# Kernel tuning notes

Hardware: AMD Instinct MI355X
Metric: run time of the kernel (lower is better)

The kernel has to match this reference:

```python
import jax, jax.numpy as jnp
import numpy as np

N_QUBITS = 20
N_LAYERS = 4
BATCH = 16
DIM = 2 ** N_QUBITS


def _apply_ry(state, theta, q, n):
    """Apply RY(theta) = [[cos(t/2), -sin(t/2)], [sin(t/2), cos(t/2)]] on qubit q.
    state: (B, 2**n) complex. Qubit 0 is most significant (qibo convention)."""
    c = jnp.cos(theta / 2).astype(state.dtype)
    s = jnp.sin(theta / 2).astype(state.dtype)
    B = state.shape[0]
    st = state.reshape(B, 2 ** q, 2, 2 ** (n - q - 1))
    a = st[:, :, 0, :]
    b = st[:, :, 1, :]
    new = jnp.stack([c * a - s * b, s * a + c * b], axis=2)
    return new.reshape(B, -1)


def _apply_cnot(state, cq, tq, n):
    """CNOT with control cq < target tq: flip target bit where control bit is 1."""
    B = state.shape[0]
    st = state.reshape(B, 2 ** cq, 2, 2 ** (tq - cq - 1), 2, 2 ** (n - tq - 1))
    ctrl0 = st[:, :, 0]                      # (B, 2^cq, mid, 2, rest)
    ctrl1 = jnp.flip(st[:, :, 1], axis=3)    # swap target |0>/<->|1>
    new = jnp.stack([ctrl0, ctrl1], axis=2)
    return new.reshape(B, -1)


def _run_circuit(state, theta):
    # theta: (N_LAYERS * N_QUBITS,) -> (N_LAYERS, N_QUBITS)
    th = theta.reshape(N_LAYERS, N_QUBITS)
    for l in range(N_LAYERS):
        for q in range(N_QUBITS):
            state = _apply_ry(state, th[l, q], q, N_QUBITS)
        for q in range(N_QUBITS - 1):
            state = _apply_cnot(state, q, q + 1, N_QUBITS)
    return state


def setup_inputs() -> dict:
    key = jax.random.key(0)
    k1, k2 = jax.random.split(key)
    x = jax.random.normal(k1, (BATCH, DIM), dtype=jnp.float32)
    theta = jax.random.normal(k2, (N_LAYERS * N_QUBITS,), dtype=jnp.float32)
    return {"x": x, "theta": theta}


def reference(x, theta):
    state = x.astype(jnp.complex64)  # initial state vector, (B, 2**n)
    state = _run_circuit(state, theta)
    return jnp.abs(state)
```

## Files before the change

kernel.cpp:

```cpp
#include <hip/hip_runtime.h>
#include <math.h>


__global__ void cs_kernel(const float* __restrict__ theta, float2* __restrict__ cs) {
    int i = threadIdx.x;
    if (i < 80) {
        float s, c;
        sincosf(theta[i] * 0.5f, &s, &c);
        cs[i] = make_float2(c, s);
    }
}

#define RYT_(TBL, MASK, Q) { float2 _sc = (TBL)[(Q)]; float _c = _sc.x, _s = _sc.y; \
  _Pragma("unroll") for (int _m = 0; _m < 32; ++_m) if (!(_m & (MASK))) { \
    float _a = v[_m], _b = v[_m | (MASK)]; \
    v[_m] = _c*_a - _s*_b; v[_m | (MASK)] = _s*_a + _c*_b; } }

#define CX_(CM, TM) { _Pragma("unroll") for (int _m = 0; _m < 32; ++_m) \
  if ((_m & (CM)) && !(_m & (TM))) { float _t = v[_m]; v[_m] = v[_m|(TM)]; v[_m|(TM)] = _t; } }

#define CXI_(COND, TM) { if (COND) { _Pragma("unroll") for (int _m = 0; _m < 32; ++_m) \
  if (!(_m & (TM))) { float _t = v[_m]; v[_m] = v[_m|(TM)]; v[_m|(TM)] = _t; } } }

__device__ __forceinline__ int mixR(int n) {
    return ((n >> 5) & 31) ^ ((n >> 10) & 1);
}
__device__ __forceinline__ int mixA(int n) {
    return ((n >> 5) & 31) ^ ((n >> 10) & 1) ^ (((n >> 11) & 1) << 3)
         ^ (((n >> 12) & 1) << 4) ^ (((n >> 13) & 1) << 4);
}
__device__ __forceinline__ int mixF(int n) {
    return ((n >> 5) & 31) ^ (((n >> 10) & 1) << 1) ^ (((n >> 11) & 1) << 2)
         ^ (((n >> 12) & 1) << 3) ^ (((n >> 13) & 1) << 4);
}
__device__ __forceinline__ int mixL(int n) {
    return ((n >> 5) & 31) ^ (((n >> 10) & 1) << 4) ^ (((n >> 11) & 1) << 2)
         ^ (((n >> 12) & 1) << 3) ^ (((n >> 13) & 1) << 4);
}

__global__ __launch_bounds__(512, 4) void pass_R(
    const float4* __restrict__ src, float4* __restrict__ dst,
    const float2* __restrict__ cs)
{
    __shared__ float lds[16384];
    const float2* csl = cs;
    int t = threadIdx.x, blk = blockIdx.x;
    int H = blk & 63, b = blk >> 6;
    int base = (b << 18) + (H << 12);
    float v[32];

#pragma unroll
    for (int i = 0; i < 8; ++i) {
        float4 w = src[base + (i << 8) + (((t >> 6) & 3) << 6) + (((t >> 8) & 1) << 11) + (t & 63)];
        v[i*4+0] = w.x; v[i*4+1] = w.y; v[i*4+2] = w.z; v[i*4+3] = w.w;
    }
    RYT_(csl, 1, 19); RYT_(csl, 2, 18); RYT_(csl, 4, 9); RYT_(csl, 8, 8); RYT_(csl, 16, 7);
    { int w1x = (t & 31) ^ ((t >> 5) & 1);
#pragma unroll
      for (int m = 0; m < 32; ++m) lds[(t << 5) | (m ^ w1x)] = v[m]; }
    __syncthreads();

    { int tp = (t & 31) | (((t >> 5) & 1) << 10) | (((t >> 6) & 7) << 11);
      int mt = mixR(tp);
#pragma unroll
      for (int f = 0; f < 32; ++f) { int fc = f << 5; v[f] = lds[(tp | fc) ^ mt ^ mixR(fc)]; }
      RYT_(csl, 1, 17); RYT_(csl, 2, 16); RYT_(csl, 4, 15); RYT_(csl, 8, 14); RYT_(csl, 16, 13);
#pragma unroll
      for (int f = 0; f < 32; ++f) { int fc = f << 5; lds[(tp | fc) ^ mt ^ mixR(fc)] = v[f]; } }
    __syncthreads();

    { int tp = ((t & 1) << 2) | (((t >> 1) & 1) << 3) | (((t >> 2) & 1) << 4)
             | (((t >> 3) & 1) << 5) | (((t >> 4) & 1) << 1) | (((t >> 5) & 1) << 0)
             | (((t >> 6) & 7) << 6);
      int mt = mixR(tp);
#pragma unroll
      for (int p = 0; p < 32; ++p) { int fc = p << 9; v[p] = lds[(tp | fc) ^ mt ^ mixR(fc)]; }
      RYT_(csl, 2, 12); RYT_(csl, 4, 11); RYT_(csl, 8, 10); RYT_(csl, 16, 6);
      int sb = base + (((t >> 6) & 7) << 6) + (t & 63);
#pragma unroll
      for (int j = 0; j < 8; ++j)
        dst[sb + (j << 9)] = make_float4(v[4*j], v[4*j+1], v[4*j+2], v[4*j+3]); }
}

template <bool FULL>
__global__ __launch_bounds__(512, 4) void pass_A(
    const float4* __restrict__ src, float4* __restrict__ dst,
    const float2* __restrict__ cs, int layer)
{
    __shared__ float lds[16384];
    const float2* csl = cs + layer * 20;
    int t = threadIdx.x, blk = blockIdx.x;
    int G = blk & 63, b = blk >> 6;
    int Gperm = ((G >> 2) & 1) | (((G >> 1) & 1) << 1) | ((G & 1) << 2) | (((G >> 3) & 7) << 3);
    float v[32];

    { int lb = (b << 18) + (((t >> 6) & 7) << 9) + (Gperm << 3) + (t & 7);
      int rg = ((t >> 3) & 7) << 12;
#pragma unroll
      for (int i = 0; i < 8; ++i) {
        float4 w = src[lb + ((i << 3) << 12) + rg];
        v[i*4+0] = w.x; v[i*4+1] = w.y; v[i*4+2] = w.z; v[i*4+3] = w.w;
      } }
    RYT_(csl, 16, 0); RYT_(csl, 8, 1); RYT_(csl, 4, 2);
    if (FULL) { RYT_(csl, 2, 12); RYT_(csl, 1, 13); }
    { int w1x = (t & 31) ^ ((t >> 5) & 1) ^ (((t >> 6) & 1) << 3)
              ^ (((t >> 7) & 1) << 4) ^ (((t >> 8) & 1) << 4);
#pragma unroll
      for (int m = 0; m < 32; ++m) lds[(t << 5) | (m ^ w1x)] = v[m]; }
    __syncthreads();

    { int tp = (t & 3) | (((t >> 2) & 1) << 7) | (((t >> 3) & 1) << 11)
             | (((t >> 4) & 1) << 12) | (((t >> 5) & 1) << 13) | (((t >> 6) & 1) << 5)
             | (((t >> 7) & 1) << 6) | (((t >> 8) & 1) << 8);
      int mt = mixA(tp);
#pragma unroll
      for (int f = 0; f < 32; ++f) {
        int fc = ((f & 1) << 9) | (((f >> 1) & 1) << 10) | (((f >> 2) & 1) << 2)
               | (((f >> 3) & 1) << 3) | (((f >> 4) & 1) << 4);
        v[f] = lds[(tp | fc) ^ mt ^ mixA(fc)]; }
      RYT_(csl, 1, 4); RYT_(csl, 2, 3);
      CX_(16, 8); CX_(8, 4); CX_(4, 2); CX_(2, 1);
#pragma unroll
      for (int f = 0; f < 32; ++f) {
        int fc = ((f & 1) << 9) | (((f >> 1) & 1) << 10) | (((f >> 2) & 1) << 2)
               | (((f >> 3) & 1) << 3) | (((f >> 4) & 1) << 4);
        lds[(tp | fc) ^ mt ^ mixA(fc)] = v[f]; } }
    __syncthreads();

    { int tp = (t & 31) | (((t >> 5) & 1) << 9) | (((t >> 6) & 1) << 10)
             | (((t >> 7) & 1) << 11) | (((t >> 8) & 1) << 12);
      int mt = mixA(tp);
#pragma unroll
      for (int f = 0; f < 32; ++f) {
        int fc = ((f & 1) << 5) | (((f >> 1) & 1) << 6) | (((f >> 2) & 1) << 7)
               | (((f >> 3) & 1) << 13) | (((f >> 4) & 1) << 8);
        v[f] = lds[(tp | fc) ^ mt ^ mixA(fc)]; }
      RYT_(csl, 16, 5);
      if (FULL) { RYT_(csl, 8, 6); RYT_(csl, 4, 7); RYT_(csl, 2, 8); RYT_(csl, 1, 9); }
      CXI_((t >> 5) & 1, 16); CX_(16, 8); CX_(8, 4); CX_(4, 2); CX_(2, 1);
#pragma unroll
      for (int f = 0; f < 32; ++f) {
        int fc = ((f & 1) << 5) | (((f >> 1) & 1) << 6) | (((f >> 2) & 1) << 7)
               | (((f >> 3) & 1) << 13) | (((f >> 4) & 1) << 8);
        lds[(tp | fc) ^ mt ^ mixA(fc)] = v[f]; } }
    __syncthreads();

    { int tp = ((t & 1) << 8) | (((t >> 1) & 1) << 9) | (((t >> 2) & 1) << 10)
             | (((t >> 3) & 1) << 6) | (((t >> 4) & 1) << 7) | (((t >> 5) & 1) << 2)
             | (((t >> 6) & 1) << 5) | (((t >> 7) & 1) << 3) | (((t >> 8) & 1) << 4);
      int mt = mixA(tp);
#pragma unroll
      for (int p = 0; p < 32; ++p) {
        int fc = ((p & 1) << 0) | (((p >> 1) & 1) << 13) | (((p >> 2) & 1) << 1)
               | (((p >> 3) & 1) << 11) | (((p >> 4) & 1) << 12);
        v[p] = lds[(tp | fc) ^ mt ^ mixA(fc)]; }
      if (FULL) { RYT_(csl, 16, 10); RYT_(csl, 8, 11); }
      CXI_((t >> 6) & 1, 16); CX_(16, 8); CX_(8, 4); CX_(4, 1);
      int sb = (b << 18) + (G << 12) + t;
#pragma unroll
      for (int j = 0; j < 8; ++j)
        dst[sb + (j << 9)] = make_float4(v[4*j], v[4*j+1], v[4*j+2], v[4*j+3]); }
}

template <bool LOWRY>
__global__ __launch_bounds__(512, 4) void pass_F(
    const float4* __restrict__ src, float4* __restrict__ dst,
    const float2* __restrict__ cs, int layer)
{
    __shared__ float lds[16384];
    const float2* csl  = cs + layer * 20;
    const float2* csl2 = cs + (layer + 1) * 20;
    int t = threadIdx.x, blk = blockIdx.x;
    int W = blk & 63, b = blk >> 6;
    int Wp = (((W >> 4) & 1) << 3) | (((W >> 5) & 1) << 4) | (((W >> 3) & 1) << 6)
           | ((W & 1) << 9) | (((W >> 1) & 1) << 10) | (((W >> 2) & 1) << 11);
    float v[32];

    { int lb = (((b << 6) | ((t >> 3) & 63)) << 12) + (t & 7) + Wp;
#pragma unroll
      for (int i = 0; i < 8; ++i) {
        float4 w = src[lb + ((i & 1) << 5) + (((i >> 1) & 1) << 7) + (((i >> 2) & 1) << 8)];
        v[i*4+0] = w.x; v[i*4+1] = w.y; v[i*4+2] = w.z; v[i*4+3] = w.w;
      } }
    RYT_(csl2, 16, 0); RYT_(csl2, 8, 1); RYT_(csl2, 4, 2); RYT_(csl2, 2, 6);
    CX_(16, 8); CX_(8, 4);
    { int w1x = (t & 31) ^ (((t >> 5) & 1) << 1) ^ (((t >> 6) & 1) << 2)
              ^ (((t >> 7) & 1) << 3) ^ (((t >> 8) & 1) << 4);
#pragma unroll
      for (int m = 0; m < 32; ++m) lds[(t << 5) | (m ^ w1x)] = v[m]; }
    __syncthreads();

    { int tp = (t & 31) | (((t >> 5) & 1) << 8) | (((t >> 6) & 1) << 5)
             | (((t >> 7) & 1) << 6) | (((t >> 8) & 1) << 7);
      int mt = mixF(tp);
#pragma unroll
      for (int f = 0; f < 32; ++f) { int fc = f << 9; v[f] = lds[(tp | fc) ^ mt ^ mixF(fc)]; }
      if (LOWRY) { RYT_(csl, 16, 14); RYT_(csl, 8, 15); RYT_(csl, 4, 16); RYT_(csl, 2, 17); RYT_(csl, 1, 18); }
      CXI_(t & 1, 16); CX_(16, 8); CX_(8, 4); CX_(4, 2); CX_(2, 1);
#pragma unroll
      for (int f = 0; f < 32; ++f) { int fc = f << 9; lds[(tp | fc) ^ mt ^ mixF(fc)] = v[f]; } }
    __syncthreads();

    { int tp = ((t & 1) << 12) | (((t >> 1) & 1) << 13) | (((t >> 2) & 1) << 0)
             | (((t >> 3) & 1) << 9) | (((t >> 4) & 1) << 10) | (((t >> 5) & 1) << 11)
             | (((t >> 6) & 1) << 2) | (((t >> 7) & 1) << 3) | (((t >> 8) & 1) << 4);
      int mt = mixF(tp);
#pragma unroll
      for (int p = 0; p < 32; ++p) {
        int fc = ((p & 1) << 8) | (((p >> 1) & 1) << 1) | (((p >> 2) & 1) << 5)
               | (((p >> 3) & 1) << 6) | (((p >> 4) & 1) << 7);
        v[p] = lds[(tp | fc) ^ mt ^ mixF(fc)]; }
      if (LOWRY) { RYT_(csl, 1, 19); }
      CXI_((t >> 3) & 1, 1);
      RYT_(csl2, 16, 3); RYT_(csl2, 8, 4); RYT_(csl2, 4, 5);
      CXI_((t >> 6) & 1, 16); CX_(16, 8); CX_(8, 4); CX_(4, 2);
      int sb = (blk << 12) + t;
#pragma unroll
      for (int j = 0; j < 8; ++j)
        dst[sb + (j << 9)] = make_float4(v[4*j], v[4*j+1], v[4*j+2], v[4*j+3]); }
}

template <bool FIN>
__global__ __launch_bounds__(512, 4) void pass_L(
    const float4* __restrict__ src, float4* __restrict__ dst,
    const float2* __restrict__ cs, int layer)
{
    __shared__ float lds[16384];
    const float2* csl = cs + layer * 20;
    int t = threadIdx.x, blk = blockIdx.x;
    int H = blk & 63, b = blk >> 6;
    int Hp = (((H >> 3) & 7) << 6) | ((H & 7) << 9);
    float v[32];

    { int rb = (b << 6) | ((t >> 6) & 7);
      int lo = Hp + (t & 63);
#pragma unroll
      for (int i = 0; i < 8; ++i) {
        float4 w = src[((rb | (i << 3)) << 12) + lo];
        v[i*4+0] = w.x; v[i*4+1] = w.y; v[i*4+2] = w.z; v[i*4+3] = w.w;
      } }
    RYT_(csl, 1, 19); RYT_(csl, 4, 9); RYT_(csl, 8, 8); RYT_(csl, 16, 7);
    { int w1x = (t & 31) ^ (((t >> 5) & 1) << 4) ^ (((t >> 6) & 1) << 2)
              ^ (((t >> 7) & 1) << 3) ^ (((t >> 8) & 1) << 4);
#pragma unroll
      for (int m = 0; m < 32; ++m) lds[(t << 5) | (m ^ w1x)] = v[m]; }
    __syncthreads();

    { int tp = (t & 3) | (((t >> 2) & 1) << 7) | (((t >> 3) & 1) << 8)
             | (((t >> 4) & 1) << 9) | (((t >> 5) & 1) << 10) | (((t >> 6) & 1) << 5)
             | (((t >> 7) & 1) << 6) | (((t >> 8) & 1) << 11);
      int mt = mixL(tp);
#pragma unroll
      for (int f = 0; f < 32; ++f) {
        int fc = ((f & 1) << 12) | (((f >> 1) & 1) << 13) | (((f >> 2) & 1) << 2)
               | (((f >> 3) & 1) << 3) | (((f >> 4) & 1) << 4);
        v[f] = lds[(tp | fc) ^ mt ^ mixL(fc)]; }
      RYT_(csl, 2, 10); RYT_(csl, 1, 11);
      CXI_((t >> 1) & 1, 16); CX_(16, 8); CX_(8, 4); CX_(4, 2); CX_(2, 1);
#pragma unroll
      for (int f = 0; f < 32; ++f) {
        int fc = ((f & 1) << 12) | (((f >> 1) & 1) << 13) | (((f >> 2) & 1) << 2)
               | (((f >> 3) & 1) << 3) | (((f >> 4) & 1) << 4);
        lds[(tp | fc) ^ mt ^ mixL(fc)] = v[f]; } }
    __syncthreads();

    { int tp = (t & 31) | (((t >> 5) & 1) << 9) | (((t >> 6) & 1) << 8)
             | (((t >> 7) & 1) << 12) | (((t >> 8) & 1) << 13);
      int mt = mixL(tp);
#pragma unroll
      for (int f = 0; f < 32; ++f) {
        int fc = ((f & 1) << 10) | (((f >> 1) & 1) << 5) | (((f >> 2) & 1) << 6)
               | (((f >> 3) & 1) << 7) | (((f >> 4) & 1) << 11);
        v[f] = lds[(tp | fc) ^ mt ^ mixL(fc)]; }
      RYT_(csl, 16, 12); RYT_(csl, 8, 13); RYT_(csl, 4, 14); RYT_(csl, 2, 15); RYT_(csl, 1, 16);
      CXI_((t >> 7) & 1, 16); CX_(16, 8); CX_(8, 4); CX_(4, 2); CX_(2, 1);
#pragma unroll
      for (int f = 0; f < 32; ++f) {
        int fc = ((f & 1) << 10) | (((f >> 1) & 1) << 5) | (((f >> 2) & 1) << 6)
               | (((f >> 3) & 1) << 7) | (((f >> 4) & 1) << 11);
        lds[(tp | fc) ^ mt ^ mixL(fc)] = v[f]; } }
    __syncthreads();

    { int tp;
      if (!FIN)
        tp = ((t & 1) << 2) | (((t >> 1) & 1) << 3) | (((t >> 2) & 1) << 4)
           | (((t >> 3) & 1) << 10) | (((t >> 4) & 1) << 5) | (((t >> 5) & 1) << 6)
           | (((t >> 6) & 1) << 1) | (((t >> 7) & 1) << 12) | (((t >> 8) & 1) << 13);
      else
        tp = ((t & 1) << 10) | (((t >> 1) & 1) << 5) | (((t >> 2) & 1) << 6)
           | (((t >> 3) & 1) << 12) | (((t >> 4) & 1) << 13) | (((t >> 5) & 1) << 2)
           | (((t >> 6) & 1) << 1) | (((t >> 7) & 1) << 3) | (((t >> 8) & 1) << 4);
      int mt = mixL(tp);
#pragma unroll
      for (int u = 0; u < 32; ++u) {
        int fc = ((u & 1) << 0) | (((u >> 1) & 1) << 8) | (((u >> 2) & 1) << 9)
               | (((u >> 3) & 1) << 7) | (((u >> 4) & 1) << 11);
        v[u] = lds[(tp | fc) ^ mt ^ mixL(fc)]; }
      RYT_(csl, 4, 17); RYT_(csl, 2, 18);
      { int e3 = FIN ? (t & 1) : ((t >> 3) & 1);
        CXI_(e3, 4); }
      CX_(4, 2); CX_(2, 1);
      if (!FIN) {
        int sb = (blk << 12) + (t & 7) + (((t >> 3) & 7) << 6)
               + (((t >> 7) & 3) << 9) + (((t >> 6) & 1) << 11);
#pragma unroll
        for (int g = 0; g < 8; ++g) {
          int bu = ((g >> 2) & 1) | (((g >> 1) & 1) << 1) | ((g & 1) << 2);
          dst[sb + (g << 3)] = make_float4(v[bu], v[bu | 8], v[bu | 16], v[bu | 24]);
        }
      } else {
        int sb = (blk << 12) + ((t & 7) << 1) + (((t >> 3) & 7) << 6)
               + (((t >> 7) & 1) << 9) + (((t >> 8) & 1) << 10) + (((t >> 6) & 1) << 11);
#pragma unroll
        for (int g = 0; g < 8; ++g) {
          int bu = ((g & 1) << 2) | (((g >> 1) & 1) << 3) | (((g >> 2) & 1) << 4);
          dst[sb + (g & 1) + (((g >> 1) & 1) << 4) + (((g >> 2) & 1) << 5)] =
            make_float4(fabsf(v[bu]), fabsf(v[bu | 1]), fabsf(v[bu | 2]), fabsf(v[bu | 3]));
        }
      } }
}

extern "C" void kernel_launch(void* const* d_in, const int* in_sizes, int n_in,
                              void* d_out, int out_size, void* d_ws, size_t ws_size,
                              hipStream_t stream) {
    const float* x     = (const float*)d_in[0];
    const float* theta = (const float*)d_in[1];
    float2* cs = (float2*)d_ws;
    float4* wsS = (float4*)((char*)d_ws + 4096);
    float4* out = (float4*)d_out;

    cs_kernel<<<1, 128, 0, stream>>>(theta, cs);

    dim3 grid(1024), block(512);
    pass_R<<<grid, block, 0, stream>>>((const float4*)x, out, cs);
    pass_A<false><<<grid, block, 0, stream>>>(out, wsS, cs, 0);
    pass_F<false><<<grid, block, 0, stream>>>(wsS, out, cs, 0);
    pass_L<false><<<grid, block, 0, stream>>>(out, wsS, cs, 1);
    pass_A<true><<<grid, block, 0, stream>>>(wsS, out, cs, 2);
    pass_F<true><<<grid, block, 0, stream>>>(out, wsS, cs, 2);
    pass_L<true><<<grid, block, 0, stream>>>(wsS, out, cs, 3);
}
```

Before: 282.1 us.

## Process two tiles per block with early prefetch of second tile

Each block now handles two 16K-element tiles: it issues global loads for both tiles up front, then runs the LDS transpose phases for the first tile while the second tile's loads are in flight, and the grid is halved to 512 blocks. __syncthreads is replaced by an explicit lgkmcnt wait plus s_barrier, so the barrier does not also wait on outstanding global loads. The intent is to hide global memory latency behind LDS work. In exchange, register pressure roughly doubles (64 floats held per thread) under launch_bounds(512,4), which risks spilling or lower occupancy, and there are fewer blocks to spread across the CUs.

```diff
diff --git a/kernel.cpp b/kernel.cpp
--- a/kernel.cpp
+++ b/kernel.cpp
@@ -11,16 +11,18 @@
     }
 }
 
-#define RYT_(TBL, MASK, Q) { float2 _sc = (TBL)[(Q)]; float _c = _sc.x, _s = _sc.y; \
+#define BAR() { asm volatile("s_waitcnt lgkmcnt(0)" ::: "memory"); __builtin_amdgcn_s_barrier(); }
+
+#define RYV_(V, TBL, MASK, Q) { float2 _sc = (TBL)[(Q)]; float _c = _sc.x, _s = _sc.y; \
   _Pragma("unroll") for (int _m = 0; _m < 32; ++_m) if (!(_m & (MASK))) { \
-    float _a = v[_m], _b = v[_m | (MASK)]; \
-    v[_m] = _c*_a - _s*_b; v[_m | (MASK)] = _s*_a + _c*_b; } }
-
-#define CX_(CM, TM) { _Pragma("unroll") for (int _m = 0; _m < 32; ++_m) \
-  if ((_m & (CM)) && !(_m & (TM))) { float _t = v[_m]; v[_m] = v[_m|(TM)]; v[_m|(TM)] = _t; } }
-
-#define CXI_(COND, TM) { if (COND) { _Pragma("unroll") for (int _m = 0; _m < 32; ++_m) \
-  if (!(_m & (TM))) { float _t = v[_m]; v[_m] = v[_m|(TM)]; v[_m|(TM)] = _t; } } }
+    float _a = (V)[_m], _b = (V)[_m | (MASK)]; \
+    (V)[_m] = _c*_a - _s*_b; (V)[_m | (MASK)] = _s*_a + _c*_b; } }
+
+#define CXV_(V, CM, TM) { _Pragma("unroll") for (int _m = 0; _m < 32; ++_m) \
+  if ((_m & (CM)) && !(_m & (TM))) { float _t = (V)[_m]; (V)[_m] = (V)[_m|(TM)]; (V)[_m|(TM)] = _t; } }
+
+#define CXIV_(V, COND, TM) { if (COND) { _Pragma("unroll") for (int _m = 0; _m < 32; ++_m) \
+  if (!(_m & (TM))) { float _t = (V)[_m]; (V)[_m] = (V)[_m|(TM)]; (V)[_m|(TM)] = _t; } } }
 
 __device__ __forceinline__ int mixR(int n) {
     return ((n >> 5) & 31) ^ ((n >> 10) & 1);
@@ -37,6 +39,34 @@
     return ((n >> 5) & 31) ^ (((n >> 10) & 1) << 4) ^ (((n >> 11) & 1) << 2)
          ^ (((n >> 12) & 1) << 3) ^ (((n >> 13) & 1) << 4);
 }
+
+#define R_LOAD(BLK, V) { int H = (BLK) & 63, b = (BLK) >> 6; \
+  int base = (b << 18) + (H << 12); \
+  _Pragma("unroll") for (int i = 0; i < 8; ++i) { \
+    float4 w = src[base + (i << 8) + (((t >> 6) & 3) << 6) + (((t >> 8) & 1) << 11) + (t & 63)]; \
+    (V)[i*4+0] = w.x; (V)[i*4+1] = w.y; (V)[i*4+2] = w.z; (V)[i*4+3] = w.w; } }
+
+#define R_PH1(V) { \
+  RYV_(V, csl, 1, 19); RYV_(V, csl, 2, 18); RYV_(V, csl, 4, 9); RYV_(V, csl, 8, 8); RYV_(V, csl, 16, 7); \
+  int w1x = (t & 31) ^ ((t >> 5) & 1); \
+  _Pragma("unroll") for (int m = 0; m < 32; ++m) lds[(t << 5) | (m ^ w1x)] = (V)[m]; }
+
+#define R_PH2(V) { int tp = (t & 31) | (((t >> 5) & 1) << 10) | (((t >> 6) & 7) << 11); \
+  int mt = mixR(tp); \
+  _Pragma("unroll") for (int f = 0; f < 32; ++f) { int fc = f << 5; (V)[f] = lds[(tp | fc) ^ mt ^ mixR(fc)]; } \
+  RYV_(V, csl, 1, 17); RYV_(V, csl, 2, 16); RYV_(V, csl, 4, 15); RYV_(V, csl, 8, 14); RYV_(V, csl, 16, 13); \
+  _Pragma("unroll") for (int f = 0; f < 32; ++f) { int fc = f << 5; lds[(tp | fc) ^ mt ^ mixR(fc)] = (V)[f]; } }
+
+#define R_PH3(V, BLK) { int tp = ((t & 1) << 2) | (((t >> 1) & 1) << 3) | (((t >> 2) & 1) << 4) \
+             | (((t >> 3) & 1) << 5) | (((t >> 4) & 1) << 1) | (((t >> 5) & 1) << 0) \
+             | (((t >> 6) & 7) << 6); \
+  int mt = mixR(tp); \
+  _Pragma("unroll") for (int p = 0; p < 32; ++p) { int fc = p << 9; (V)[p] = lds[(tp | fc) ^ mt ^ mixR(fc)]; } \
+  RYV_(V, csl, 2, 12); RYV_(V, csl, 4, 11); RYV_(V, csl, 8, 10); RYV_(V, csl, 16, 6); \
+  int H = (BLK) & 63, b = (BLK) >> 6; \
+  int sb = (b << 18) + (H << 12) + (((t >> 6) & 7) << 6) + (t & 63); \
+  _Pragma("unroll") for (int j = 0; j < 8; ++j) \
+    dst[sb + (j << 9)] = make_float4((V)[4*j], (V)[4*j+1], (V)[4*j+2], (V)[4*j+3]); }
 
 __global__ __launch_bounds__(512, 4) void pass_R(
     const float4* __restrict__ src, float4* __restrict__ dst,
@@ -44,43 +74,78 @@
 {
     __shared__ float lds[16384];
     const float2* csl = cs;
-    int t = threadIdx.x, blk = blockIdx.x;
-    int H = blk & 63, b = blk >> 6;
-    int base = (b << 18) + (H << 12);
-    float v[32];
-
-#pragma unroll
-    for (int i = 0; i < 8; ++i) {
-        float4 w = src[base + (i << 8) + (((t >> 6) & 3) << 6) + (((t >> 8) & 1) << 11) + (t & 63)];
-        v[i*4+0] = w.x; v[i*4+1] = w.y; v[i*4+2] = w.z; v[i*4+3] = w.w;
-    }
-    RYT_(csl, 1, 19); RYT_(csl, 2, 18); RYT_(csl, 4, 9); RYT_(csl, 8, 8); RYT_(csl, 16, 7);
-    { int w1x = (t & 31) ^ ((t >> 5) & 1);
-#pragma unroll
-      for (int m = 0; m < 32; ++m) lds[(t << 5) | (m ^ w1x)] = v[m]; }
-    __syncthreads();
-
-    { int tp = (t & 31) | (((t >> 5) & 1) << 10) | (((t >> 6) & 7) << 11);
-      int mt = mixR(tp);
-#pragma unroll
-      for (int f = 0; f < 32; ++f) { int fc = f << 5; v[f] = lds[(tp | fc) ^ mt ^ mixR(fc)]; }
-      RYT_(csl, 1, 17); RYT_(csl, 2, 16); RYT_(csl, 4, 15); RYT_(csl, 8, 14); RYT_(csl, 16, 13);
-#pragma unroll
-      for (int f = 0; f < 32; ++f) { int fc = f << 5; lds[(tp | fc) ^ mt ^ mixR(fc)] = v[f]; } }
-    __syncthreads();
-
-    { int tp = ((t & 1) << 2) | (((t >> 1) & 1) << 3) | (((t >> 2) & 1) << 4)
-             | (((t >> 3) & 1) << 5) | (((t >> 4) & 1) << 1) | (((t >> 5) & 1) << 0)
-             | (((t >> 6) & 7) << 6);
-      int mt = mixR(tp);
-#pragma unroll
-      for (int p = 0; p < 32; ++p) { int fc = p << 9; v[p] = lds[(tp | fc) ^ mt ^ mixR(fc)]; }
-      RYT_(csl, 2, 12); RYT_(csl, 4, 11); RYT_(csl, 8, 10); RYT_(csl, 16, 6);
-      int sb = base + (((t >> 6) & 7) << 6) + (t & 63);
-#pragma unroll
-      for (int j = 0; j < 8; ++j)
-        dst[sb + (j << 9)] = make_float4(v[4*j], v[4*j+1], v[4*j+2], v[4*j+3]); }
-}
+    int t = threadIdx.x;
+    int blk0 = blockIdx.x, blk1 = blockIdx.x + 512;
+    float va[32], vb[32];
+
+    R_LOAD(blk0, va); R_LOAD(blk1, vb);
+    R_PH1(va); BAR();
+    R_PH2(va); BAR();
+    R_PH3(va, blk0); BAR();
+    R_PH1(vb); BAR();
+    R_PH2(vb); BAR();
+    R_PH3(vb, blk1);
+}
+
+#define A_LOAD(BLK, V) { int G = (BLK) & 63, b = (BLK) >> 6; \
+  int Gperm = ((G >> 2) & 1) | (((G >> 1) & 1) << 1) | ((G & 1) << 2) | (((G >> 3) & 7) << 3); \
+  int lb = (b << 18) + (((t >> 6) & 7) << 9) + (Gperm << 3) + (t & 7); \
+  int rg = ((t >> 3) & 7) << 12; \
+  _Pragma("unroll") for (int i = 0; i < 8; ++i) { \
+    float4 w = src[lb + ((i << 3) << 12) + rg]; \
+    (V)[i*4+0] = w.x; (V)[i*4+1] = w.y; (V)[i*4+2] = w.z; (V)[i*4+3] = w.w; } }
+
+#define A_PH1(V) { \
+  RYV_(V, csl, 16, 0); RYV_(V, csl, 8, 1); RYV_(V, csl, 4, 2); \
+  if (FULL) { RYV_(V, csl, 2, 12); RYV_(V, csl, 1, 13); } \
+  int w1x = (t & 31) ^ ((t >> 5) & 1) ^ (((t >> 6) & 1) << 3) \
+          ^ (((t >> 7) & 1) << 4) ^ (((t >> 8) & 1) << 4); \
+  _Pragma("unroll") for (int m = 0; m < 32; ++m) lds[(t << 5) | (m ^ w1x)] = (V)[m]; }
+
+#define A_PH2(V) { int tp = (t & 3) | (((t >> 2) & 1) << 7) | (((t >> 3) & 1) << 11) \
+             | (((t >> 4) & 1) << 12) | (((t >> 5) & 1) << 13) | (((t >> 6) & 1) << 5) \
+             | (((t >> 7) & 1) << 6) | (((t >> 8) & 1) << 8); \
+  int mt = mixA(tp); \
+  _Pragma("unroll") for (int f = 0; f < 32; ++f) { \
+    int fc = ((f & 1) << 9) | (((f >> 1) & 1) << 10) | (((f >> 2) & 1) << 2) \
+           | (((f >> 3) & 1) << 3) | (((f >> 4) & 1) << 4); \
+    (V)[f] = lds[(tp | fc) ^ mt ^ mixA(fc)]; } \
+  RYV_(V, csl, 1, 4); RYV_(V, csl, 2, 3); \
+  CXV_(V, 16, 8); CXV_(V, 8, 4); CXV_(V, 4, 2); CXV_(V, 2, 1); \
+  _Pragma("unroll") for (int f = 0; f < 32; ++f) { \
+    int fc = ((f & 1) << 9) | (((f >> 1) & 1) << 10) | (((f >> 2) & 1) << 2) \
+           | (((f >> 3) & 1) << 3) | (((f >> 4) & 1) << 4); \
+    lds[(tp | fc) ^ mt ^ mixA(fc)] = (V)[f]; } }
+
+#define A_PH3(V) { int tp = (t & 31) | (((t >> 5) & 1) << 9) | (((t >> 6) & 1) << 10) \
+             | (((t >> 7) & 1) << 11) | (((t >> 8) & 1) << 12); \
+  int mt = mixA(tp); \
+  _Pragma("unroll") for (int f = 0; f < 32; ++f) { \
+    int fc = ((f & 1) << 5) | (((f >> 1) & 1) << 6) | (((f >> 2) & 1) << 7) \
+           | (((f >> 3) & 1) << 13) | (((f >> 4) & 1) << 8); \
+    (V)[f] = lds[(tp | fc) ^ mt ^ mixA(fc)]; } \
+  RYV_(V, csl, 16, 5); \
+  if (FULL) { RYV_(V, csl, 8, 6); RYV_(V, csl, 4, 7); RYV_(V, csl, 2, 8); RYV_(V, csl, 1, 9); } \
+  CXIV_(V, (t >> 5) & 1, 16); CXV_(V, 16, 8); CXV_(V, 8, 4); CXV_(V, 4, 2); CXV_(V, 2, 1); \
+  _Pragma("unroll") for (int f = 0; f < 32; ++f) { \
+    int fc = ((f & 1) << 5) | (((f >> 1) & 1) << 6) | (((f >> 2) & 1) << 7) \
+           | (((f >> 3) & 1) << 13) | (((f >> 4) & 1) << 8); \
+    lds[(tp | fc) ^ mt ^ mixA(fc)] = (V)[f]; } }
+
+#define A_PH4(V, BLK) { int tp = ((t & 1) << 8) | (((t >> 1) & 1) << 9) | (((t >> 2) & 1) << 10) \
+             | (((t >> 3) & 1) << 6) | (((t >> 4) & 1) << 7) | (((t >> 5) & 1) << 2) \
+             | (((t >> 6) & 1) << 5) | (((t >> 7) & 1) << 3) | (((t >> 8) & 1) << 4); \
+  int mt = mixA(tp); \
+  _Pragma("unroll") for (int p = 0; p < 32; ++p) { \
+    int fc = ((p & 1) << 0) | (((p >> 1) & 1) << 13) | (((p >> 2) & 1) << 1) \
+           | (((p >> 3) & 1) << 11) | (((p >> 4) & 1) << 12); \
+    (V)[p] = lds[(tp | fc) ^ mt ^ mixA(fc)]; } \
+  if (FULL) { RYV_(V, csl, 16, 10); RYV_(V, csl, 8, 11); } \
+  CXIV_(V, (t >> 6) & 1, 16); CXV_(V, 16, 8); CXV_(V, 8, 4); CXV_(V, 4, 1); \
+  int G = (BLK) & 63, b = (BLK) >> 6; \
+  int sb = (b << 18) + (G << 12) + t; \
+  _Pragma("unroll") for (int j = 0; j < 8; ++j) \
+    dst[sb + (j << 9)] = make_float4((V)[4*j], (V)[4*j+1], (V)[4*j+2], (V)[4*j+3]); }
 
 template <bool FULL>
 __global__ __launch_bounds__(512, 4) void pass_A(
@@ -89,78 +154,59 @@
 {
     __shared__ float lds[16384];
     const float2* csl = cs + layer * 20;
-    int t = threadIdx.x, blk = blockIdx.x;
-    int G = blk & 63, b = blk >> 6;
-    int Gperm = ((G >> 2) & 1) | (((G >> 1) & 1) << 1) | ((G & 1) << 2) | (((G >> 3) & 7) << 3);
-    float v[32];
-
-    { int lb = (b << 18) + (((t >> 6) & 7) << 9) + (Gperm << 3) + (t & 7);
-      int rg = ((t >> 3) & 7) << 12;
-#pragma unroll
-      for (int i = 0; i < 8; ++i) {
-        float4 w = src[lb + ((i << 3) << 12) + rg];
-        v[i*4+0] = w.x; v[i*4+1] = w.y; v[i*4+2] = w.z; v[i*4+3] = w.w;
-      } }
-    RYT_(csl, 16, 0); RYT_(csl, 8, 1); RYT_(csl, 4, 2);
-    if (FULL) { RYT_(csl, 2, 12); RYT_(csl, 1, 13); }
-    { int w1x = (t & 31) ^ ((t >> 5) & 1) ^ (((t >> 6) & 1) << 3)
-              ^ (((t >> 7) & 1) << 4) ^ (((t >> 8) & 1) << 4);
-#pragma unroll
-      for (int m = 0; m < 32; ++m) lds[(t << 5) | (m ^ w1x)] = v[m]; }
-    __syncthreads();
-
-    { int tp = (t & 3) | (((t >> 2) & 1) << 7) | (((t >> 3) & 1) << 11)
-             | (((t >> 4) & 1) << 12) | (((t >> 5) & 1) << 13) | (((t >> 6) & 1) << 5)
-             | (((t >> 7) & 1) << 6) | (((t >> 8) & 1) << 8);
-      int mt = mixA(tp);
-#pragma unroll
-      for (int f = 0; f < 32; ++f) {
-        int fc = ((f & 1) << 9) | (((f >> 1) & 1) << 10) | (((f >> 2) & 1) << 2)
-               | (((f >> 3) & 1) << 3) | (((f >> 4) & 1) << 4);
-        v[f] = lds[(tp | fc) ^ mt ^ mixA(fc)]; }
-      RYT_(csl, 1, 4); RYT_(csl, 2, 3);
-      CX_(16, 8); CX_(8, 4); CX_(4, 2); CX_(2, 1);
-#pragma unroll
-      for (int f = 0; f < 32; ++f) {
-        int fc = ((f & 1) << 9) | (((f >> 1) & 1) << 10) | (((f >> 2) & 1) << 2)
-               | (((f >> 3) & 1) << 3) | (((f >> 4) & 1) << 4);
-        lds[(tp | fc) ^ mt ^ mixA(fc)] = v[f]; } }
-    __syncthreads();
-
-    { int tp = (t & 31) | (((t >> 5) & 1) << 9) | (((t >> 6) & 1) << 10)
-             | (((t >> 7) & 1) << 11) | (((t >> 8) & 1) << 12);
-      int mt = mixA(tp);
-#pragma unroll
-      for (int f = 0; f < 32; ++f) {
-        int fc = ((f & 1) << 5) | (((f >> 1) & 1) << 6) | (((f >> 2) & 1) << 7)
-               | (((f >> 3) & 1) << 13) | (((f >> 4) & 1) << 8);
-        v[f] = lds[(tp | fc) ^ mt ^ mixA(fc)]; }
-      RYT_(csl, 16, 5);
-      if (FULL) { RYT_(csl, 8, 6); RYT_(csl, 4, 7); RYT_(csl, 2, 8); RYT_(csl, 1, 9); }
-      CXI_((t >> 5) & 1, 16); CX_(16, 8); CX_(8, 4); CX_(4, 2); CX_(2, 1);
-#pragma unroll
-      for (int f = 0; f < 32; ++f) {
-        int fc = ((f & 1) << 5) | (((f >> 1) & 1) << 6) | (((f >> 2) & 1) << 7)
-               | (((f >> 3) & 1) << 13) | (((f >> 4) & 1) << 8);
-        lds[(tp | fc) ^ mt ^ mixA(fc)] = v[f]; } }
-    __syncthreads();
-
-    { int tp = ((t & 1) << 8) | (((t >> 1) & 1) << 9) | (((t >> 2) & 1) << 10)
-             | (((t >> 3) & 1) << 6) | (((t >> 4) & 1) << 7) | (((t >> 5) & 1) << 2)
-             | (((t >> 6) & 1) << 5) | (((t >> 7) & 1) << 3) | (((t >> 8) & 1) << 4);
-      int mt = mixA(tp);
-#pragma unroll
-      for (int p = 0; p < 32; ++p) {
-        int fc = ((p & 1) << 0) | (((p >> 1) & 1) << 13) | (((p >> 2) & 1) << 1)
-               | (((p >> 3) & 1) << 11) | (((p >> 4) & 1) << 12);
-        v[p] = lds[(tp | fc) ^ mt ^ mixA(fc)]; }
-      if (FULL) { RYT_(csl, 16, 10); RYT_(csl, 8, 11); }
-      CXI_((t >> 6) & 1, 16); CX_(16, 8); CX_(8, 4); CX_(4, 1);
-      int sb = (b << 18) + (G << 12) + t;
-#pragma unroll
-      for (int j = 0; j < 8; ++j)
-        dst[sb + (j << 9)] = make_float4(v[4*j], v[4*j+1], v[4*j+2], v[4*j+3]); }
-}
+    int t = threadIdx.x;
+    int blk0 = blockIdx.x, blk1 = blockIdx.x + 512;
+    float va[32], vb[32];
+
+    A_LOAD(blk0, va); A_LOAD(blk1, vb);
+    A_PH1(va); BAR();
+    A_PH2(va); BAR();
+    A_PH3(va); BAR();
+    A_PH4(va, blk0); BAR();
+    A_PH1(vb); BAR();
+    A_PH2(vb); BAR();
+    A_PH3(vb); BAR();
+    A_PH4(vb, blk1);
+}
+
+#define F_LOAD(BLK, V) { int W = (BLK) & 63, b = (BLK) >> 6; \
+  int Wp = (((W >> 4) & 1) << 3) | (((W >> 5) & 1) << 4) | (((W >> 3) & 1) << 6) \
+         | ((W & 1) << 9) | (((W >> 1) & 1) << 10) | (((W >> 2) & 1) << 11); \
+  int lb = (((b << 6) | ((t >> 3) & 63)) << 12) + (t & 7) + Wp; \
+  _Pragma("unroll") for (int i = 0; i < 8; ++i) { \
+    float4 w = src[lb + ((i & 1) << 5) + (((i >> 1) & 1) << 7) + (((i >> 2) & 1) << 8)]; \
+    (V)[i*4+0] = w.x; (V)[i*4+1] = w.y; (V)[i*4+2] = w.z; (V)[i*4+3] = w.w; } }
+
+#define F_PH1(V) { \
+  RYV_(V, csl2, 16, 0); RYV_(V, csl2, 8, 1); RYV_(V, csl2, 4, 2); RYV_(V, csl2, 2, 6); \
+  CXV_(V, 16, 8); CXV_(V, 8, 4); \
+  int w1x = (t & 31) ^ (((t >> 5) & 1) << 1) ^ (((t >> 6) & 1) << 2) \
+          ^ (((t >> 7) & 1) << 3) ^ (((t >> 8) & 1) << 4); \
+  _Pragma("unroll") for (int m = 0; m < 32; ++m) lds[(t << 5) | (m ^ w1x)] = (V)[m]; }
+
+#define F_PH2(V) { int tp = (t & 31) | (((t >> 5) & 1) << 8) | (((t >> 6) & 1) << 5) \
+             | (((t >> 7) & 1) << 6) | (((t >> 8) & 1) << 7); \
+  int mt = mixF(tp); \
+  _Pragma("unroll") for (int f = 0; f < 32; ++f) { int fc = f << 9; (V)[f] = lds[(tp | fc) ^ mt ^ mixF(fc)]; } \
+  if (LOWRY) { RYV_(V, csl, 16, 14); RYV_(V, csl, 8, 15); RYV_(V, csl, 4, 16); RYV_(V, csl, 2, 17); RYV_(V, csl, 1, 18); } \
+  CXIV_(V, t & 1, 16); CXV_(V, 16, 8); CXV_(V, 8, 4); CXV_(V, 4, 2); CXV_(V, 2, 1); \
+  _Pragma("unroll") for (int f = 0; f < 32; ++f) { int fc = f << 9; lds[(tp | fc) ^ mt ^ mixF(fc)] = (V)[f]; } }
+
+#define F_PH3(V, BLK) { int tp = ((t & 1) << 12) | (((t >> 1) & 1) << 13) | (((t >> 2) & 1) << 0) \
+             | (((t >> 3) & 1) << 9) | (((t >> 4) & 1) << 10) | (((t >> 5) & 1) << 11) \
+             | (((t >> 6) & 1) << 2) | (((t >> 7) & 1) << 3) | (((t >> 8) & 1) << 4); \
+  int mt = mixF(tp); \
+  _Pragma("unroll") for (int p = 0; p < 32; ++p) { \
+    int fc = ((p & 1) << 8) | (((p >> 1) & 1) << 1) | (((p >> 2) & 1) << 5) \
+           | (((p >> 3) & 1) << 6) | (((p >> 4) & 1) << 7); \
+    (V)[p] = lds[(tp | fc) ^ mt ^ mixF(fc)]; } \
+  if (LOWRY) { RYV_(V, csl, 1, 19); } \
+  CXIV_(V, (t >> 3) & 1, 1); \
+  RYV_(V, csl2, 16, 3); RYV_(V, csl2, 8, 4); RYV_(V, csl2, 4, 5); \
+  CXIV_(V, (t >> 6) & 1, 16); CXV_(V, 16, 8); CXV_(V, 8, 4); CXV_(V, 4, 2); \
+  int sb = ((BLK) << 12) + t; \
+  _Pragma("unroll") for (int j = 0; j < 8; ++j) \
+    dst[sb + (j << 9)] = make_float4((V)[4*j], (V)[4*j+1], (V)[4*j+2], (V)[4*j+3]); }
 
 template <bool LOWRY>
 __global__ __launch_bounds__(512, 4) void pass_F(
@@ -170,55 +216,96 @@
     __shared__ float lds[16384];
     const float2* csl  = cs + layer * 20;
     const float2* csl2 = cs + (layer + 1) * 20;
-    int t = threadIdx.x, blk = blockIdx.x;
-    int W = blk & 63, b = blk >> 6;
-    int Wp = (((W >> 4) & 1) << 3) | (((W >> 5) & 1) << 4) | (((W >> 3) & 1) << 6)
-           | ((W & 1) << 9) | (((W >> 1) & 1) << 10) | (((W >> 2) & 1) << 11);
-    float v[32];
-
-    { int lb = (((b << 6) | ((t >> 3) & 63)) << 12) + (t & 7) + Wp;
-#pragma unroll
-      for (int i = 0; i < 8; ++i) {
-        float4 w = src[lb + ((i & 1) << 5) + (((i >> 1) & 1) << 7) + (((i >> 2) & 1) << 8)];
-        v[i*4+0] = w.x; v[i*4+1] = w.y; v[i*4+2] = w.z; v[i*4+3] = w.w;
-      } }
-    RYT_(csl2, 16, 0); RYT_(csl2, 8, 1); RYT_(csl2, 4, 2); RYT_(csl2, 2, 6);
-    CX_(16, 8); CX_(8, 4);
-    { int w1x = (t & 31) ^ (((t >> 5) & 1) << 1) ^ (((t >> 6) & 1) << 2)
-              ^ (((t >> 7) & 1) << 3) ^ (((t >> 8) & 1) << 4);
-#pragma unroll
-      for (int m = 0; m < 32; ++m) lds[(t << 5) | (m ^ w1x)] = v[m]; }
-    __syncthreads();
-
-    { int tp = (t & 31) | (((t >> 5) & 1) << 8) | (((t >> 6) & 1) << 5)
-             | (((t >> 7) & 1) << 6) | (((t >> 8) & 1) << 7);
-      int mt = mixF(tp);
-#pragma unroll
-      for (int f = 0; f < 32; ++f) { int fc = f << 9; v[f] = lds[(tp | fc) ^ mt ^ mixF(fc)]; }
-      if (LOWRY) { RYT_(csl, 16, 14); RYT_(csl, 8, 15); RYT_(csl, 4, 16); RYT_(csl, 2, 17); RYT_(csl, 1, 18); }
-      CXI_(t & 1, 16); CX_(16, 8); CX_(8, 4); CX_(4, 2); CX_(2, 1);
-#pragma unroll
-      for (int f = 0; f < 32; ++f) { int fc = f << 9; lds[(tp | fc) ^ mt ^ mixF(fc)] = v[f]; } }
-    __syncthreads();
-
-    { int tp = ((t & 1) << 12) | (((t >> 1) & 1) << 13) | (((t >> 2) & 1) << 0)
-             | (((t >> 3) & 1) << 9) | (((t >> 4) & 1) << 10) | (((t >> 5) & 1) << 11)
-             | (((t >> 6) & 1) << 2) | (((t >> 7) & 1) << 3) | (((t >> 8) & 1) << 4);
-      int mt = mixF(tp);
-#pragma unroll
-      for (int p = 0; p < 32; ++p) {
-        int fc = ((p & 1) << 8) | (((p >> 1) & 1) << 1) | (((p >> 2) & 1) << 5)
-               | (((p >> 3) & 1) << 6) | (((p >> 4) & 1) << 7);
-        v[p] = lds[(tp | fc) ^ mt ^ mixF(fc)]; }
-      if (LOWRY) { RYT_(csl, 1, 19); }
-      CXI_((t >> 3) & 1, 1);
-      RYT_(csl2, 16, 3); RYT_(csl2, 8, 4); RYT_(csl2, 4, 5);
-      CXI_((t >> 6) & 1, 16); CX_(16, 8); CX_(8, 4); CX_(4, 2);
-      int sb = (blk << 12) + t;
-#pragma unroll
-      for (int j = 0; j < 8; ++j)
-        dst[sb + (j << 9)] = make_float4(v[4*j], v[4*j+1], v[4*j+2], v[4*j+3]); }
-}
+    int t = threadIdx.x;
+    int blk0 = blockIdx.x, blk1 = blockIdx.x + 512;
+    float va[32], vb[32];
+
+    F_LOAD(blk0, va); F_LOAD(blk1, vb);
+    F_PH1(va); BAR();
+    F_PH2(va); BAR();
+    F_PH3(va, blk0); BAR();
+    F_PH1(vb); BAR();
+    F_PH2(vb); BAR();
+    F_PH3(vb, blk1);
+}
+
+#define L_LOAD(BLK, V) { int H = (BLK) & 63, b = (BLK) >> 6; \
+  int Hp = (((H >> 3) & 7) << 6) | ((H & 7) << 9); \
+  int rb = (b << 6) | ((t >> 6) & 7); \
+  int lo = Hp + (t & 63); \
+  _Pragma("unroll") for (int i = 0; i < 8; ++i) { \
+    float4 w = src[((rb | (i << 3)) << 12) + lo]; \
+    (V)[i*4+0] = w.x; (V)[i*4+1] = w.y; (V)[i*4+2] = w.z; (V)[i*4+3] = w.w; } }
+
+#define L_PH1(V) { \
+  RYV_(V, csl, 1, 19); RYV_(V, csl, 4, 9); RYV_(V, csl, 8, 8); RYV_(V, csl, 16, 7); \
+  int w1x = (t & 31) ^ (((t >> 5) & 1) << 4) ^ (((t >> 6) & 1) << 2) \
+          ^ (((t >> 7) & 1) << 3) ^ (((t >> 8) & 1) << 4); \
+  _Pragma("unroll") for (int m = 0; m < 32; ++m) lds[(t << 5) | (m ^ w1x)] = (V)[m]; }
+
+#define L_PH2(V) { int tp = (t & 3) | (((t >> 2) & 1) << 7) | (((t >> 3) & 1) << 8) \
+             | (((t >> 4) & 1) << 9) | (((t >> 5) & 1) << 10) | (((t >> 6) & 1) << 5) \
+             | (((t >> 7) & 1) << 6) | (((t >> 8) & 1) << 11); \
+  int mt = mixL(tp); \
+  _Pragma("unroll") for (int f = 0; f < 32; ++f) { \
+    int fc = ((f & 1) << 12) | (((f >> 1) & 1) << 13) | (((f >> 2) & 1) << 2) \
+           | (((f >> 3) & 1) << 3) | (((f >> 4) & 1) << 4); \
+    (V)[f] = lds[(tp | fc) ^ mt ^ mixL(fc)]; } \
+  RYV_(V, csl, 2, 10); RYV_(V, csl, 1, 11); \
+  CXIV_(V, (t >> 1) & 1, 16); CXV_(V, 16, 8); CXV_(V, 8, 4); CXV_(V, 4, 2); CXV_(V, 2, 1); \
+  _Pragma("unroll") for (int f = 0; f < 32; ++f) { \
+    int fc = ((f & 1) << 12) | (((f >> 1) & 1) << 13) | (((f >> 2) & 1) << 2) \
+           | (((f >> 3) & 1) << 3) | (((f >> 4) & 1) << 4); \
+    lds[(tp | fc) ^ mt ^ mixL(fc)] = (V)[f]; } }
+
+#define L_PH3(V) { int tp = (t & 31) | (((t >> 5) & 1) << 9) | (((t >> 6) & 1) << 8) \
+             | (((t >> 7) & 1) << 12) | (((t >> 8) & 1) << 13); \
+  int mt = mixL(tp); \
+  _Pragma("unroll") for (int f = 0; f < 32; ++f) { \
+    int fc = ((f & 1) << 10) | (((f >> 1) & 1) << 5) | (((f >> 2) & 1) << 6) \
+           | (((f >> 3) & 1) << 7) | (((f >> 4) & 1) << 11); \
+    (V)[f] = lds[(tp | fc) ^ mt ^ mixL(fc)]; } \
+  RYV_(V, csl, 16, 12); RYV_(V, csl, 8, 13); RYV_(V, csl, 4, 14); RYV_(V, csl, 2, 15); RYV_(V, csl, 1, 16); \
+  CXIV_(V, (t >> 7) & 1, 16); CXV_(V, 16, 8); CXV_(V, 8, 4); CXV_(V, 4, 2); CXV_(V, 2, 1); \
+  _Pragma("unroll") for (int f = 0; f < 32; ++f) { \
+    int fc = ((f & 1) << 10) | (((f >> 1) & 1) << 5) | (((f >> 2) & 1) << 6) \
+           | (((f >> 3) & 1) << 7) | (((f >> 4) & 1) << 11); \
+    lds[(tp | fc) ^ mt ^ mixL(fc)] = (V)[f]; } }
+
+#define L_PH4(V, BLK) { int tp; \
+  if (!FIN) \
+    tp = ((t & 1) << 2) | (((t >> 1) & 1) << 3) | (((t >> 2) & 1) << 4) \
+       | (((t >> 3) & 1) << 10) | (((t >> 4) & 1) << 5) | (((t >> 5) & 1) << 6) \
+       | (((t >> 6) & 1) << 1) | (((t >> 7) & 1) << 12) | (((t >> 8) & 1) << 13); \
+  else \
+    tp = ((t & 1) << 10) | (((t >> 1) & 1) << 5) | (((t >> 2) & 1) << 6) \
+       | (((t >> 3) & 1) << 12) | (((t >> 4) & 1) << 13) | (((t >> 5) & 1) << 2) \
+       | (((t >> 6) & 1) << 1) | (((t >> 7) & 1) << 3) | (((t >> 8) & 1) << 4); \
+  int mt = mixL(tp); \
+  _Pragma("unroll") for (int u = 0; u < 32; ++u) { \
+    int fc = ((u & 1) << 0) | (((u >> 1) & 1) << 8) | (((u >> 2) & 1) << 9) \
+           | (((u >> 3) & 1) << 7) | (((u >> 4) & 1) << 11); \
+    (V)[u] = lds[(tp | fc) ^ mt ^ mixL(fc)]; } \
+  RYV_(V, csl, 4, 17); RYV_(V, csl, 2, 18); \
+  { int e3 = FIN ? (t & 1) : ((t >> 3) & 1); \
+    CXIV_(V, e3, 4); } \
+  CXV_(V, 4, 2); CXV_(V, 2, 1); \
+  if (!FIN) { \
+    int sb = ((BLK) << 12) + (t & 7) + (((t >> 3) & 7) << 6) \
+           + (((t >> 7) & 3) << 9) + (((t >> 6) & 1) << 11); \
+    _Pragma("unroll") for (int g = 0; g < 8; ++g) { \
+      int bu = ((g >> 2) & 1) | (((g >> 1) & 1) << 1) | ((g & 1) << 2); \
+      dst[sb + (g << 3)] = make_float4((V)[bu], (V)[bu | 8], (V)[bu | 16], (V)[bu | 24]); \
+    } \
+  } else { \
+    int sb = ((BLK) << 12) + ((t & 7) << 1) + (((t >> 3) & 7) << 6) \
+           + (((t >> 7) & 1) << 9) + (((t >> 8) & 1) << 10) + (((t >> 6) & 1) << 11); \
+    _Pragma("unroll") for (int g = 0; g < 8; ++g) { \
+      int bu = ((g & 1) << 2) | (((g >> 1) & 1) << 3) | (((g >> 2) & 1) << 4); \
+      dst[sb + (g & 1) + (((g >> 1) & 1) << 4) + (((g >> 2) & 1) << 5)] = \
+        make_float4(fabsf((V)[bu]), fabsf((V)[bu | 1]), fabsf((V)[bu | 2]), fabsf((V)[bu | 3])); \
+    } \
+  } }
 
 template <bool FIN>
 __global__ __launch_bounds__(512, 4) void pass_L(
@@ -227,97 +314,19 @@
 {
     __shared__ float lds[16384];
     const float2* csl = cs + layer * 20;
-    int t = threadIdx.x, blk = blockIdx.x;
-    int H = blk & 63, b = blk >> 6;
-    int Hp = (((H >> 3) & 7) << 6) | ((H & 7) << 9);
-    float v[32];
-
-    { int rb = (b << 6) | ((t >> 6) & 7);
-      int lo = Hp + (t & 63);
-#pragma unroll
-      for (int i = 0; i < 8; ++i) {
-        float4 w = src[((rb | (i << 3)) << 12) + lo];
-        v[i*4+0] = w.x; v[i*4+1] = w.y; v[i*4+2] = w.z; v[i*4+3] = w.w;
-      } }
-    RYT_(csl, 1, 19); RYT_(csl, 4, 9); RYT_(csl, 8, 8); RYT_(csl, 16, 7);
-    { int w1x = (t & 31) ^ (((t >> 5) & 1) << 4) ^ (((t >> 6) & 1) << 2)
-              ^ (((t >> 7) & 1) << 3) ^ (((t >> 8) & 1) << 4);
-#pragma unroll
-      for (int m = 0; m < 32; ++m) lds[(t << 5) | (m ^ w1x)] = v[m]; }
-    __syncthreads();
-
-    { int tp = (t & 3) | (((t >> 2) & 1) << 7) | (((t >> 3) & 1) << 8)
-             | (((t >> 4) & 1) << 9) | (((t >> 5) & 1) << 10) | (((t >> 6) & 1) << 5)
-             | (((t >> 7) & 1) << 6) | (((t >> 8) & 1) << 11);
-      int mt = mixL(tp);
-#pragma unroll
-      for (int f = 0; f < 32; ++f) {
-        int fc = ((f & 1) << 12) | (((f >> 1) & 1) << 13) | (((f >> 2) & 1) << 2)
-               | (((f >> 3) & 1) << 3) | (((f >> 4) & 1) << 4);
-        v[f] = lds[(tp | fc) ^ mt ^ mixL(fc)]; }
-      RYT_(csl, 2, 10); RYT_(csl, 1, 11);
-      CXI_((t >> 1) & 1, 16); CX_(16, 8); CX_(8, 4); CX_(4, 2); CX_(2, 1);
-#pragma unroll
-      for (int f = 0; f < 32; ++f) {
-        int fc = ((f & 1) << 12) | (((f >> 1) & 1) << 13) | (((f >> 2) & 1) << 2)
-               | (((f >> 3) & 1) << 3) | (((f >> 4) & 1) << 4);
-        lds[(tp | fc) ^ mt ^ mixL(fc)] = v[f]; } }
-    __syncthreads();
-
-    { int tp = (t & 31) | (((t >> 5) & 1) << 9) | (((t >> 6) & 1) << 8)
-             | (((t >> 7) & 1) << 12) | (((t >> 8) & 1) << 13);
-      int mt = mixL(tp);
-#pragma unroll
-      for (int f = 0; f < 32; ++f) {
-        int fc = ((f & 1) << 10) | (((f >> 1) & 1) << 5) | (((f >> 2) & 1) << 6)
-               | (((f >> 3) & 1) << 7) | (((f >> 4) & 1) << 11);
-        v[f] = lds[(tp | fc) ^ mt ^ mixL(fc)]; }
-      RYT_(csl, 16, 12); RYT_(csl, 8, 13); RYT_(csl, 4, 14); RYT_(csl, 2, 15); RYT_(csl, 1, 16);
-      CXI_((t >> 7) & 1, 16); CX_(16, 8); CX_(8, 4); CX_(4, 2); CX_(2, 1);
-#pragma unroll
-      for (int f = 0; f < 32; ++f) {
-        int fc = ((f & 1) << 10) | (((f >> 1) & 1) << 5) | (((f >> 2) & 1) << 6)
-               | (((f >> 3) & 1) << 7) | (((f >> 4) & 1) << 11);
-        lds[(tp | fc) ^ mt ^ mixL(fc)] = v[f]; } }
-    __syncthreads();
-
-    { int tp;
-      if (!FIN)
-        tp = ((t & 1) << 2) | (((t >> 1) & 1) << 3) | (((t >> 2) & 1) << 4)
-           | (((t >> 3) & 1) << 10) | (((t >> 4) & 1) << 5) | (((t >> 5) & 1) << 6)
-           | (((t >> 6) & 1) << 1) | (((t >> 7) & 1) << 12) | (((t >> 8) & 1) << 13);
-      else
-        tp = ((t & 1) << 10) | (((t >> 1) & 1) << 5) | (((t >> 2) & 1) << 6)
-           | (((t >> 3) & 1) << 12) | (((t >> 4) & 1) << 13) | (((t >> 5) & 1) << 2)
-           | (((t >> 6) & 1) << 1) | (((t >> 7) & 1) << 3) | (((t >> 8) & 1) << 4);
-      int mt = mixL(tp);
-#pragma unroll
-      for (int u = 0; u < 32; ++u) {
-        int fc = ((u & 1) << 0) | (((u >> 1) & 1) << 8) | (((u >> 2) & 1) << 9)
-               | (((u >> 3) & 1) << 7) | (((u >> 4) & 1) << 11);
-        v[u] = lds[(tp | fc) ^ mt ^ mixL(fc)]; }
-      RYT_(csl, 4, 17); RYT_(csl, 2, 18);
-      { int e3 = FIN ? (t & 1) : ((t >> 3) & 1);
-        CXI_(e3, 4); }
-      CX_(4, 2); CX_(2, 1);
-      if (!FIN) {
-        int sb = (blk << 12) + (t & 7) + (((t >> 3) & 7) << 6)
-               + (((t >> 7) & 3) << 9) + (((t >> 6) & 1) << 11);
-#pragma unroll
-        for (int g = 0; g < 8; ++g) {
-          int bu = ((g >> 2) & 1) | (((g >> 1) & 1) << 1) | ((g & 1) << 2);
-          dst[sb + (g << 3)] = make_float4(v[bu], v[bu | 8], v[bu | 16], v[bu | 24]);
-        }
-      } else {
-        int sb = (blk << 12) + ((t & 7) << 1) + (((t >> 3) & 7) << 6)
-               + (((t >> 7) & 1) << 9) + (((t >> 8) & 1) << 10) + (((t >> 6) & 1) << 11);
-#pragma unroll
-        for (int g = 0; g < 8; ++g) {
-          int bu = ((g & 1) << 2) | (((g >> 1) & 1) << 3) | (((g >> 2) & 1) << 4);
-          dst[sb + (g & 1) + (((g >> 1) & 1) << 4) + (((g >> 2) & 1) << 5)] =
-            make_float4(fabsf(v[bu]), fabsf(v[bu | 1]), fabsf(v[bu | 2]), fabsf(v[bu | 3]));
-        }
-      } }
+    int t = threadIdx.x;
+    int blk0 = blockIdx.x, blk1 = blockIdx.x + 512;
+    float va[32], vb[32];
+
+    L_LOAD(blk0, va); L_LOAD(blk1, vb);
+    L_PH1(va); BAR();
+    L_PH2(va); BAR();
+    L_PH3(va); BAR();
+    L_PH4(va, blk0); BAR();
+    L_PH1(vb); BAR();
+    L_PH2(vb); BAR();
+    L_PH3(vb); BAR();
+    L_PH4(vb, blk1);
 }
 
 extern "C" void kernel_launch(void* const* d_in, const int* in_sizes, int n_in,
@@ -331,7 +340,7 @@
 
     cs_kernel<<<1, 128, 0, stream>>>(theta, cs);
 
-    dim3 grid(1024), block(512);
+    dim3 grid(512), block(512);
     pass_R<<<grid, block, 0, stream>>>((const float4*)x, out, cs);
     pass_A<false><<<grid, block, 0, stream>>>(out, wsS, cs, 0);
     pass_F<false><<<grid, block, 0, stream>>>(wsS, out, cs, 0);
```

Result: slower. 555.4 us (+96.9%).
